# Kernel optimization log

Measured on AMD Instinct MI355X. Metric: run time of the kernel, lower is better.

The kernel has to match this reference:

```python
import jax, jax.numpy as jnp
import numpy as np

GRID = 32
SCALE_FACTOR = 0.2
EPS = 1e-12


def _compute_phi(verts, faces, G):
    """Unsigned distance-to-mesh on a GxGxG grid over [-1,1]^3, zeroed outside the mesh.
    Returns phi[z, y, x] (grid_sample D,H,W layout). verts [V,3], faces [F,3] int.
    Matches the SDF CUDA kernel semantics: phi = penetration depth (dist inside, 0 outside)."""
    v0 = verts[faces[:, 0]]  # [F,3]
    v1 = verts[faces[:, 1]]
    v2 = verts[faces[:, 2]]
    e0 = v1 - v0             # [F,3]
    e1 = v2 - v0
    a = jnp.sum(e0 * e0, -1)             # [F]
    b = jnp.sum(e0 * e1, -1)
    c = jnp.sum(e1 * e1, -1)

    lin = jnp.linspace(-1.0, 1.0, G, dtype=verts.dtype)
    zz, yy, xx = jnp.meshgrid(lin, lin, lin, indexing='ij')
    pts = jnp.stack([xx, yy, zz], -1).reshape(-1, 3)   # [P,3], coords (x,y,z), P=G^3

    # --- point-to-triangle squared distance, all [P,F] after one [P,F,3] temp ---
    w = pts[:, None, :] - v0[None, :, :]               # [P,F,3]
    f = jnp.sum(w * w, -1)                             # |p-v0|^2   [P,F]
    de0 = jnp.sum(w * e0, -1)                          # (p-v0).e0  [P,F]
    de1 = jnp.sum(w * e1, -1)                          # (p-v0).e1  [P,F]

    det = a * c - b * b                                # [F]
    det_s = jnp.where(det > EPS, det, 1.0)
    u = (c * de0 - b * de1) / det_s                    # barycentric of plane projection
    v = (a * de1 - b * de0) / det_s
    inside_tri = (u >= 0) & (v >= 0) & (u + v <= 1) & (det > EPS)
    plane_d2 = f - (u * de0 + v * de1)                 # squared dist to plane point

    # edge v0->v1
    a_s = jnp.where(a > EPS, a, 1.0)
    t0 = jnp.clip(de0 / a_s, 0.0, 1.0)
    d2_0 = f - 2.0 * t0 * de0 + t0 * t0 * a
    # edge v0->v2
    c_s = jnp.where(c > EPS, c, 1.0)
    t1 = jnp.clip(de1 / c_s, 0.0, 1.0)
    d2_1 = f - 2.0 * t1 * de1 + t1 * t1 * c
    # edge v1->v2: e2 = e1-e0; w1 = p - v1 = w - e0
    ee2 = a + c - 2.0 * b                              # |e2|^2
    ee2_s = jnp.where(ee2 > EPS, ee2, 1.0)
    dot2 = de1 - de0 - (b - a)                         # w1.e2
    w1sq = f - 2.0 * de0 + a                           # |w1|^2
    t2 = jnp.clip(dot2 / ee2_s, 0.0, 1.0)
    d2_2 = w1sq - 2.0 * t2 * dot2 + t2 * t2 * ee2

    edge_d2 = jnp.minimum(jnp.minimum(d2_0, d2_1), d2_2)
    d2 = jnp.where(inside_tri, plane_d2, edge_d2)
    d2 = jnp.maximum(d2, 0.0)
    dist = jnp.sqrt(jnp.min(d2, axis=1))               # [P]

    # --- inside/outside via +z ray casting parity ---
    x0, y0, z0 = v0[:, 0], v0[:, 1], v0[:, 2]
    x1, y1, z1 = v1[:, 0], v1[:, 1], v1[:, 2]
    x2, y2, z2 = v2[:, 0], v2[:, 1], v2[:, 2]
    det2 = (x1 - x0) * (y2 - y0) - (x2 - x0) * (y1 - y0)   # [F]
    det2_s = jnp.where(jnp.abs(det2) > EPS, det2, 1.0)
    px = pts[:, 0:1]; py = pts[:, 1:2]; pz = pts[:, 2:3]   # [P,1]
    u2 = ((px - x0) * (y2 - y0) - (py - y0) * (x2 - x0)) / det2_s  # [P,F]
    v2b = ((x1 - x0) * (py - y0) - (y1 - y0) * (px - x0)) / det2_s
    in2d = (u2 >= 0) & (v2b >= 0) & (u2 + v2b <= 1) & (jnp.abs(det2) > EPS)
    zint = z0 + u2 * (z1 - z0) + v2b * (z2 - z0)
    hits = jnp.sum((in2d & (zint > pz)).astype(jnp.int32), axis=1)  # [P]
    inside_mesh = (hits % 2).astype(dist.dtype)

    phi = dist * inside_mesh                           # >= 0 everywhere
    return phi.reshape(G, G, G)                        # [z, y, x]


def _trilinear_zeros(phi, q):
    """torch grid_sample(mode=bilinear, padding=zeros, align_corners=True) on a
    [G,G,G] (z,y,x) volume at points q [N,3] with coords (x,y,z) in [-1,1]."""
    G = phi.shape[0]
    fidx = (q + 1.0) * 0.5 * (G - 1)                   # [N,3] float indices (x,y,z)
    i0 = jnp.floor(fidx).astype(jnp.int32)
    w1 = fidx - i0.astype(fidx.dtype)
    w0 = 1.0 - w1
    out = jnp.zeros(q.shape[0], dtype=phi.dtype)
    for dz in (0, 1):
        for dy in (0, 1):
            for dx in (0, 1):
                ix = i0[:, 0] + dx
                iy = i0[:, 1] + dy
                iz = i0[:, 2] + dz
                valid = (ix >= 0) & (ix < G) & (iy >= 0) & (iy < G) & (iz >= 0) & (iz < G)
                val = phi[jnp.clip(iz, 0, G - 1), jnp.clip(iy, 0, G - 1), jnp.clip(ix, 0, G - 1)]
                wgt = ((w1[:, 0] if dx else w0[:, 0]) *
                       (w1[:, 1] if dy else w0[:, 1]) *
                       (w1[:, 2] if dz else w0[:, 2]))
                out = out + jnp.where(valid, val * wgt, 0.0)
    return out


def _sdf_loss(human_verts, object_verts, faces):
    sg = jax.lax.stop_gradient
    # bounding boxes (computed under no_grad in the original)
    bmin_h = jnp.min(human_verts, axis=0); bmax_h = jnp.max(human_verts, axis=0)
    bmin_o = jnp.min(object_verts, axis=0); bmax_o = jnp.max(object_verts, axis=0)
    overlap = jnp.all(bmin_h <= bmax_o) & jnp.all(bmin_o <= bmax_h)

    center = sg(0.5 * (bmin_h + bmax_h))                               # [3]
    scale = sg((1.0 + SCALE_FACTOR) * 0.5 * jnp.max(bmax_h - bmin_h))  # scalar

    hv_scaled = sg((human_verts - center) / scale)      # in [-1,1]^3 by construction
    phi = sg(_compute_phi(hv_scaled, faces, GRID))      # [G,G,G], no_grad in original

    q = (object_verts - center) / scale                 # grads flow to object_verts
    phi_val = _trilinear_zeros(phi, q)                  # [N]
    loss = jnp.sum(phi_val) ** 2
    return jnp.where(overlap, loss, jnp.zeros((), dtype=loss.dtype))


def setup_inputs() -> dict:
    key = jax.random.key(0)
    k1, k2, k3 = jax.random.split(key, 3)
    human_verts = jax.random.normal(k1, (778, 3), dtype=jnp.float32)
    object_verts = jax.random.normal(k2, (4096, 3), dtype=jnp.float32)
    faces = jax.random.randint(k3, (1538, 3), 0, 778, dtype=jnp.int32)
    return {"human_verts": human_verts, "object_verts": object_verts, "faces": faces}


def reference(human_verts, object_verts, faces):
    return _sdf_loss(human_verts, object_verts, faces)
```

## Files before the change

### kernel.cpp

```cpp
#include <hip/hip_runtime.h>

#define EPSF 1e-12f
#define GN 32
#define NPTS (GN * GN * GN)
#define NCOL (GN * GN)
#define FSPLIT 16
#define NCG 16
#define NBLK (NCG * FSPLIT)
#define NTHR 1024
#define MAXCH 160
#define CAP 8192
#define POISON 0xAAAAAAAAu

__device__ __forceinline__ float dot_rn(const float* x, const float* y) {
    return __fadd_rn(__fadd_rn(__fmul_rn(x[0], y[0]), __fmul_rn(x[1], y[1])),
                     __fmul_rn(x[2], y[2]));
}
__device__ __forceinline__ float wmin64(float v) {
    for (int o = 32; o > 0; o >>= 1) v = fminf(v, __shfl_xor(v, o));
    return v;
}
__device__ __forceinline__ float wmax64(float v) {
    for (int o = 32; o > 0; o >>= 1) v = fmaxf(v, __shfl_xor(v, o));
    return v;
}
__device__ __forceinline__ float wsum64(float v) {
    for (int o = 32; o > 0; o >>= 1) v += __shfl_xor(v, o);
    return v;
}
__device__ __forceinline__ float gridc(int g) {
    return __fadd_rn(-1.0f, __fmul_rn((float)g, 2.0f / 31.0f));
}
__device__ __forceinline__ int clampi(int v, int lo, int hi) {
    return v < lo ? lo : (v > hi ? hi : v);
}

__device__ __forceinline__ void frec(const float* __restrict__ hv,
                                     const int* __restrict__ faces, int f,
                                     float cx, float cy, float cz, float sc,
                                     float* o) {
    const float qnan = __int_as_float(0x7FC00000);
    int ia = faces[3 * f + 0], ib = faces[3 * f + 1], ic = faces[3 * f + 2];
    float v0[3], v1[3], v2[3];
    for (int k = 0; k < 3; ++k) {
        float cen = (k == 0) ? cx : ((k == 1) ? cy : cz);
        v0[k] = __fdiv_rn(__fsub_rn(hv[3 * ia + k], cen), sc);
        v1[k] = __fdiv_rn(__fsub_rn(hv[3 * ib + k], cen), sc);
        v2[k] = __fdiv_rn(__fsub_rn(hv[3 * ic + k], cen), sc);
    }
    float e0[3], e1[3];
    for (int k = 0; k < 3; ++k) {
        e0[k] = __fsub_rn(v1[k], v0[k]);
        e1[k] = __fsub_rn(v2[k], v0[k]);
    }
    float a = dot_rn(e0, e0);
    float b = dot_rn(e0, e1);
    float cc = dot_rn(e1, e1);
    float det = __fsub_rn(__fmul_rn(a, cc), __fmul_rn(b, b));
    float inv_det = (det > EPSF) ? (1.0f / det) : qnan;
    float inv_a = 1.0f / ((a > EPSF) ? a : 1.0f);
    float inv_c = 1.0f / ((cc > EPSF) ? cc : 1.0f);
    float ee2 = __fsub_rn(__fadd_rn(a, cc), __fmul_rn(2.0f, b));
    float inv_ee2 = 1.0f / ((ee2 > EPSF) ? ee2 : 1.0f);
    float det2 = __fsub_rn(__fmul_rn(e0[0], e1[1]), __fmul_rn(e1[0], e0[1]));
    float inv_det2s = (fabsf(det2) > EPSF) ? (1.0f / det2) : qnan;
    o[0] = v0[0]; o[1] = v0[1]; o[2] = v0[2];
    o[3] = e0[0]; o[4] = e0[1]; o[5] = e0[2];
    o[6] = e1[0]; o[7] = e1[1]; o[8] = e1[2];
    o[9] = a; o[10] = b; o[11] = cc;
    o[12] = inv_det; o[13] = inv_a; o[14] = inv_c;
    o[15] = ee2; o[16] = inv_ee2; o[17] = inv_det2s;
    o[18] = __fsub_rn(b, a); o[19] = 0.f;
}

__device__ __forceinline__ float celld2(const float* r, float px, float py, float pz) {
    float wx = __fsub_rn(px, r[0]), wy = __fsub_rn(py, r[1]), wz = __fsub_rn(pz, r[2]);
    float ff = wx * wx + wy * wy + wz * wz;
    float de0 = wx * r[3] + wy * r[4] + wz * r[5];
    float de1 = wx * r[6] + wy * r[7] + wz * r[8];
    float u = (r[11] * de0 - r[10] * de1) * r[12];
    float v = (r[9] * de1 - r[10] * de0) * r[12];
    bool inside = (u >= 0.0f) & (v >= 0.0f) & (u + v <= 1.0f);
    float plane_d2 = ff - (u * de0 + v * de1);
    float t0 = fminf(fmaxf(de0 * r[13], 0.0f), 1.0f);
    float d2_0 = ff + t0 * (t0 * r[9] - 2.0f * de0);
    float t1 = fminf(fmaxf(de1 * r[14], 0.0f), 1.0f);
    float d2_1 = ff + t1 * (t1 * r[11] - 2.0f * de1);
    float dot2 = (de1 - de0) - r[18];
    float w1sq = ff - 2.0f * de0 + r[9];
    float t2 = fminf(fmaxf(dot2 * r[16], 0.0f), 1.0f);
    float d2_2 = w1sq + t2 * (t2 * r[15] - 2.0f * dot2);
    float ed2 = fminf(fminf(d2_0, d2_1), d2_2);
    float d2 = inside ? plane_d2 : ed2;
    return fmaxf(d2, 0.0f);
}

__global__ void __launch_bounds__(NTHR) k_all(
    const float* __restrict__ hv, int nh,
    const float* __restrict__ ov, int no,
    const int* __restrict__ faces, int nf,
    unsigned* __restrict__ d2u, unsigned* __restrict__ parm,
    unsigned* __restrict__ counter, float* __restrict__ out)
{
    __shared__ float s_fd[MAXCH * 20];
    __shared__ unsigned s_sm[NCOL];
    __shared__ unsigned s_clist[CAP];
    __shared__ unsigned s_cnt[16];
    __shared__ unsigned s_pm[64];
    __shared__ float s_w[16][12];
    __shared__ float s_hdr[4];
    __shared__ float s_hb[6];
    __shared__ float s_ovl;
    __shared__ unsigned s_last;

    int t = threadIdx.x, lane = t & 63, wvid = t >> 6;
    int fs = blockIdx.x >> 4;
    int cg = blockIdx.x & 15;
    const float step = 2.0f / 31.0f;

    for (int i = t; i < NCOL; i += NTHR) s_sm[i] = 0u;
    if (t < 64) s_pm[t] = 0u;

    {
        float mnx = INFINITY, mny = INFINITY, mnz = INFINITY;
        float mxx = -INFINITY, mxy = -INFINITY, mxz = -INFINITY;
        for (int i = t; i < nh; i += NTHR) {
            float x = hv[3 * i], y = hv[3 * i + 1], z = hv[3 * i + 2];
            mnx = fminf(mnx, x); mny = fminf(mny, y); mnz = fminf(mnz, z);
            mxx = fmaxf(mxx, x); mxy = fmaxf(mxy, y); mxz = fmaxf(mxz, z);
        }
        mnx = wmin64(mnx); mny = wmin64(mny); mnz = wmin64(mnz);
        mxx = wmax64(mxx); mxy = wmax64(mxy); mxz = wmax64(mxz);
        if (lane == 0) {
            s_w[wvid][0] = mnx; s_w[wvid][1] = mny; s_w[wvid][2] = mnz;
            s_w[wvid][3] = mxx; s_w[wvid][4] = mxy; s_w[wvid][5] = mxz;
        }
        __syncthreads();
        if (wvid == 0) {
            float a0 = (lane < 16) ? s_w[lane][0] : INFINITY;
            float a1 = (lane < 16) ? s_w[lane][1] : INFINITY;
            float a2 = (lane < 16) ? s_w[lane][2] : INFINITY;
            float a3 = (lane < 16) ? s_w[lane][3] : -INFINITY;
            float a4 = (lane < 16) ? s_w[lane][4] : -INFINITY;
            float a5 = (lane < 16) ? s_w[lane][5] : -INFINITY;
            a0 = wmin64(a0); a1 = wmin64(a1); a2 = wmin64(a2);
            a3 = wmax64(a3); a4 = wmax64(a4); a5 = wmax64(a5);
            if (lane == 0) {
                float e0 = __fsub_rn(a3, a0);
                float e1 = __fsub_rn(a4, a1);
                float e2 = __fsub_rn(a5, a2);
                float m = fmaxf(e0, fmaxf(e1, e2));
                s_hdr[0] = __fmul_rn(0.5f, __fadd_rn(a0, a3));
                s_hdr[1] = __fmul_rn(0.5f, __fadd_rn(a1, a4));
                s_hdr[2] = __fmul_rn(0.5f, __fadd_rn(a2, a5));
                s_hdr[3] = __fmul_rn(0.6f, m);
                s_hb[0] = a0; s_hb[1] = a1; s_hb[2] = a2;
                s_hb[3] = a3; s_hb[4] = a4; s_hb[5] = a5;
            }
        }
        __syncthreads();
    }
    float cx = s_hdr[0], cy = s_hdr[1], cz = s_hdr[2], sc = s_hdr[3];

    int chunkB = (nf + FSPLIT - 1) / FSPLIT;
    int f0B = fs * chunkB;
    int nloc = min(nf, f0B + chunkB) - f0B;
    for (int i = t; i < nloc; i += NTHR)
        frec(hv, faces, f0B + i, cx, cy, cz, sc, s_fd + i * 20);
    {
        float onx = INFINITY, ony = INFINITY, onz = INFINITY;
        float oxx = -INFINITY, oxy = -INFINITY, oxz = -INFINITY;
        for (int j = t; j < no; j += NTHR) {
            float x = ov[3 * j + 0], y = ov[3 * j + 1], z = ov[3 * j + 2];
            onx = fminf(onx, x); ony = fminf(ony, y); onz = fminf(onz, z);
            oxx = fmaxf(oxx, x); oxy = fmaxf(oxy, y); oxz = fmaxf(oxz, z);
            float qx = __fdiv_rn(__fsub_rn(x, cx), sc);
            float qy = __fdiv_rn(__fsub_rn(y, cy), sc);
            float qz = __fdiv_rn(__fsub_rn(z, cz), sc);
            float fx = __fmul_rn(__fmul_rn(__fadd_rn(qx, 1.0f), 0.5f), 31.0f);
            float fy = __fmul_rn(__fmul_rn(__fadd_rn(qy, 1.0f), 0.5f), 31.0f);
            float fz = __fmul_rn(__fmul_rn(__fadd_rn(qz, 1.0f), 0.5f), 31.0f);
            int ix0 = (int)floorf(fx), iy0 = (int)floorf(fy), iz0 = (int)floorf(fz);
            unsigned zb = 0u;
            if ((iz0 >= 0) & (iz0 < GN)) zb |= 1u << iz0;
            if ((iz0 + 1 >= 0) & (iz0 + 1 < GN)) zb |= 1u << (iz0 + 1);
            if (zb) {
                for (int dy = 0; dy < 2; ++dy)
                    for (int dx = 0; dx < 2; ++dx) {
                        int ix = ix0 + dx, iy = iy0 + dy;
                        if ((ix >= 0) & (ix < GN) & (iy >= 0) & (iy < GN))
                            atomicOr(&s_sm[iy * GN + ix], zb);
                    }
            }
        }
        onx = wmin64(onx); ony = wmin64(ony); onz = wmin64(onz);
        oxx = wmax64(oxx); oxy = wmax64(oxy); oxz = wmax64(oxz);
        if (lane == 0) {
            s_w[wvid][6] = onx; s_w[wvid][7] = ony; s_w[wvid][8] = onz;
            s_w[wvid][9] = oxx; s_w[wvid][10] = oxy; s_w[wvid][11] = oxz;
        }
    }
    __syncthreads();
    if (t == 0) {
        float a0 = INFINITY, a1 = INFINITY, a2 = INFINITY;
        float a3 = -INFINITY, a4 = -INFINITY, a5 = -INFINITY;
        for (int wv = 0; wv < 16; ++wv) {
            a0 = fminf(a0, s_w[wv][6]); a1 = fminf(a1, s_w[wv][7]);
            a2 = fminf(a2, s_w[wv][8]); a3 = fmaxf(a3, s_w[wv][9]);
            a4 = fmaxf(a4, s_w[wv][10]); a5 = fmaxf(a5, s_w[wv][11]);
        }
        bool ovl = (s_hb[0] <= a3) && (s_hb[1] <= a4) && (s_hb[2] <= a5) &&
                   (a0 <= s_hb[3]) && (a1 <= s_hb[4]) && (a2 <= s_hb[5]);
        s_ovl = ovl ? 1.0f : 0.0f;
    }

    {
        int col = cg * 64 + lane;
        int gx = col & 31, gy = col >> 5;
        float px = __fadd_rn(-1.0f, __fmul_rn((float)gx, step));
        float py = __fadd_rn(-1.0f, __fmul_rn((float)gy, step));
        int i0 = __builtin_amdgcn_readfirstlane((wvid * nloc) / 16);
        int i1 = __builtin_amdgcn_readfirstlane(((wvid + 1) * nloc) / 16);

        unsigned cmask = 0u;
        for (int i = i0; i < i1; ++i) {
            const float* q = s_fd + i * 20;
            float v0x = q[0], v0y = q[1], v0z = q[2];
            float e0x = q[3], e0y = q[4], e0z = q[5];
            float e1x = q[6], e1y = q[7], e1z = q[8];
            float inv_det2s = q[17];

            float wx = __fsub_rn(px, v0x), wy = __fsub_rn(py, v0y);
            float u2n = __fsub_rn(__fmul_rn(wx, e1y), __fmul_rn(wy, e1x));
            float v2n = __fsub_rn(__fmul_rn(e0x, wy), __fmul_rn(e0y, wx));
            float u2 = __fmul_rn(u2n, inv_det2s);
            float v2 = __fmul_rn(v2n, inv_det2s);
            bool in2d = (u2 >= 0.0f) & (v2 >= 0.0f) & (__fadd_rn(u2, v2) <= 1.0f);
            float zint = __fadd_rn(__fadd_rn(v0z, __fmul_rn(u2, e0z)), __fmul_rn(v2, e1z));
            int c = 0;
            {
                float p;
                p = __fadd_rn(-1.0f, __fmul_rn((float)(15), step));      if (zint > p) c = 16;
                p = __fadd_rn(-1.0f, __fmul_rn((float)(c + 7), step));   if (zint > p) c += 8;
                p = __fadd_rn(-1.0f, __fmul_rn((float)(c + 3), step));   if (zint > p) c += 4;
                p = __fadd_rn(-1.0f, __fmul_rn((float)(c + 1), step));   if (zint > p) c += 2;
                p = __fadd_rn(-1.0f, __fmul_rn((float)(c), step));       if (zint > p) c += 1;
                p = __fadd_rn(-1.0f, __fmul_rn((float)(c), step));       if (zint > p) c += 1;
            }
            unsigned mask = (c == 0) ? 0u : (0xffffffffu >> (32 - c));
            cmask ^= in2d ? mask : 0u;
        }
        atomicXor(&s_pm[lane], cmask);
        __syncthreads();
        if (t < 64) atomicXor(&parm[cg * 64 + t], s_pm[t]);
    }

    unsigned nc;
    {
        unsigned cnt = 0;
        for (int chunk = wvid * 32; chunk < wvid * 32 + 32; ++chunk) {
            unsigned cid = (unsigned)(chunk * 64 + lane);
            bool present = (s_sm[cid >> 5] >> (cid & 31u)) & 1u;
            cnt += (unsigned)__popcll(__ballot(present));
        }
        if (lane == 0) s_cnt[wvid] = cnt;
        __syncthreads();
        unsigned base = 0;
        for (int wv = 0; wv < wvid; ++wv) base += s_cnt[wv];
        nc = base;
        for (int wv = wvid; wv < 16; ++wv) nc += s_cnt[wv];
        if (nc <= CAP) {
            for (int chunk = wvid * 32; chunk < wvid * 32 + 32; ++chunk) {
                unsigned cid = (unsigned)(chunk * 64 + lane);
                bool present = (s_sm[cid >> 5] >> (cid & 31u)) & 1u;
                unsigned long long bal = __ballot(present);
                unsigned pre = (unsigned)__popcll(bal & ((1ull << lane) - 1ull));
                if (present) s_clist[base + pre] = cid;
                base += (unsigned)__popcll(bal);
            }
        }
        __syncthreads();
    }

    {
        bool uselist = nc <= CAP;
        unsigned nbatch = uselist ? ((nc + 63) >> 6) : (NPTS / 64);
        for (unsigned cb = (unsigned)cg + 16u * (unsigned)wvid; cb < nbatch;
             cb += 256u) {
            unsigned idx = cb * 64 + (unsigned)lane;
            bool cvalid; unsigned cid;
            if (uselist) { cvalid = idx < nc; cid = cvalid ? s_clist[idx] : 0u; }
            else { cid = idx; cvalid = (s_sm[cid >> 5] >> (cid & 31u)) & 1u; }
            int gx = (int)((cid >> 5) & 31u), gy = (int)(cid >> 10),
                gz = (int)(cid & 31u);
            float px = gridc(gx), py = gridc(gy), pz = gridc(gz);
            float dmin = 3.402823466e38f;
            for (int i = 0; i < nloc; ++i)
                dmin = fminf(dmin, celld2(s_fd + i * 20, px, py, pz));
            if (cvalid) atomicMin(&d2u[cid], __float_as_uint(dmin));
        }
    }

    __syncthreads();
    if (t == 0) {
        unsigned old = atomicAdd(counter, 1u);
        s_last = (old == POISON + (unsigned)(NBLK - 1)) ? 1u : 0u;
    }
    __syncthreads();
    if (s_last == 0u) return;

    {
        float ovl = s_ovl;
        s_sm[t] = __hip_atomic_load(&parm[t], __ATOMIC_RELAXED,
                                    __HIP_MEMORY_SCOPE_AGENT) ^ POISON;
        __syncthreads();
        float acc = 0.0f;
        for (int j = t; j < no; j += NTHR) {
            float qx = __fdiv_rn(__fsub_rn(ov[3 * j + 0], cx), sc);
            float qy = __fdiv_rn(__fsub_rn(ov[3 * j + 1], cy), sc);
            float qz = __fdiv_rn(__fsub_rn(ov[3 * j + 2], cz), sc);
            float fx = __fmul_rn(__fmul_rn(__fadd_rn(qx, 1.0f), 0.5f), 31.0f);
            float fy = __fmul_rn(__fmul_rn(__fadd_rn(qy, 1.0f), 0.5f), 31.0f);
            float fz = __fmul_rn(__fmul_rn(__fadd_rn(qz, 1.0f), 0.5f), 31.0f);
            float flx = floorf(fx), fly = floorf(fy), flz = floorf(fz);
            int ix0 = (int)flx, iy0 = (int)fly, iz0 = (int)flz;
            float w1x = __fsub_rn(fx, flx), w0x = __fsub_rn(1.0f, w1x);
            float w1y = __fsub_rn(fy, fly), w0y = __fsub_rn(1.0f, w1y);
            float w1z = __fsub_rn(fz, flz), w0z = __fsub_rn(1.0f, w1z);
            int xc0 = clampi(ix0, 0, 31), xc1 = clampi(ix0 + 1, 0, 31);
            int yc0 = clampi(iy0, 0, 31), yc1 = clampi(iy0 + 1, 0, 31);
            int zc0 = clampi(iz0, 0, 31), zc1 = clampi(iz0 + 1, 0, 31);
            unsigned du[8];
#pragma unroll
            for (int k = 0; k < 8; ++k) {
                int xx = (k & 1) ? xc1 : xc0;
                int yy = ((k >> 1) & 1) ? yc1 : yc0;
                int zz = (k >> 2) ? zc1 : zc0;
                du[k] = __hip_atomic_load(&d2u[(yy * GN + xx) * GN + zz],
                            __ATOMIC_RELAXED, __HIP_MEMORY_SCOPE_AGENT);
            }
            for (int dy = 0; dy < 2; ++dy)
                for (int dx = 0; dx < 2; ++dx) {
                    int ix = ix0 + dx, iy = iy0 + dy;
                    bool okxy = (ix >= 0) & (ix < GN) & (iy >= 0) & (iy < GN);
                    unsigned pm = okxy ? s_sm[iy * GN + ix] : 0u;
                    for (int dz = 0; dz < 2; ++dz) {
                        int iz = iz0 + dz;
                        bool ok = okxy & (iz >= 0) & (iz < GN);
                        if (ok && ((pm >> iz) & 1u)) {
                            float val = sqrtf(__uint_as_float(du[dz * 4 + dy * 2 + dx]));
                            float wgt = __fmul_rn(
                                __fmul_rn(dx ? w1x : w0x, dy ? w1y : w0y),
                                dz ? w1z : w0z);
                            acc = __fadd_rn(acc, __fmul_rn(val, wgt));
                        }
                    }
                }
        }
        acc = wsum64(acc);
        if (lane == 0) s_w[wvid][0] = acc;
        __syncthreads();
        if (wvid == 0) {
            float v = (lane < 16) ? s_w[lane][0] : 0.0f;
            v = wsum64(v);
            if (lane == 0) {
                float loss = __fmul_rn(v, v);
                out[0] = (ovl != 0.0f) ? loss : 0.0f;
            }
        }
    }
}

extern "C" void kernel_launch(void* const* d_in, const int* in_sizes, int n_in,
                              void* d_out, int out_size, void* d_ws, size_t ws_size,
                              hipStream_t stream) {
    const float* hv = (const float*)d_in[0];
    const float* ov = (const float*)d_in[1];
    const int* faces = (const int*)d_in[2];
    int nh = in_sizes[0] / 3;
    int no = in_sizes[1] / 3;
    int nf = in_sizes[2] / 3;

    unsigned* d2u = (unsigned*)d_ws;
    unsigned* parm = d2u + NPTS;
    unsigned* counter = parm + NCOL;

    k_all<<<NBLK, NTHR, 0, stream>>>(hv, nh, ov, no, faces, nf,
                                     d2u, parm, counter, (float*)d_out);
}
```

Before: 112.5 us.

## Split face chunk across waves per cell batch and reduce minima in LDS

Each wave used to own whole batches of 64 cells and loop over every face in the block's chunk. Now all 16 waves work on the same cell batch, each taking one sixteenth of the faces. Partial minima are combined with LDS atomicMin, then written to global memory with one atomicMin per cell. The aim is to balance work across waves when there are few cell batches, and to cut global atomics. The cost is extra block-wide barriers per group of eight batches, plus LDS atomic traffic.

```diff
diff --git a/kernel.cpp b/kernel.cpp
--- a/kernel.cpp
+++ b/kernel.cpp
@@ -10,6 +10,7 @@
 #define NTHR 1024
 #define MAXCH 160
 #define CAP 8192
+#define LB 8
 #define POISON 0xAAAAAAAAu
 
 __device__ __forceinline__ float dot_rn(const float* x, const float* y) {
@@ -107,6 +108,7 @@
     __shared__ unsigned s_clist[CAP];
     __shared__ unsigned s_cnt[16];
     __shared__ unsigned s_pm[64];
+    __shared__ unsigned s_dm[LB * 64];
     __shared__ float s_w[16][12];
     __shared__ float s_hdr[4];
     __shared__ float s_hb[6];
@@ -285,19 +287,44 @@
     {
         bool uselist = nc <= CAP;
         unsigned nbatch = uselist ? ((nc + 63) >> 6) : (NPTS / 64);
-        for (unsigned cb = (unsigned)cg + 16u * (unsigned)wvid; cb < nbatch;
-             cb += 256u) {
-            unsigned idx = cb * 64 + (unsigned)lane;
-            bool cvalid; unsigned cid;
-            if (uselist) { cvalid = idx < nc; cid = cvalid ? s_clist[idx] : 0u; }
-            else { cid = idx; cvalid = (s_sm[cid >> 5] >> (cid & 31u)) & 1u; }
-            int gx = (int)((cid >> 5) & 31u), gy = (int)(cid >> 10),
-                gz = (int)(cid & 31u);
-            float px = gridc(gx), py = gridc(gy), pz = gridc(gz);
-            float dmin = 3.402823466e38f;
-            for (int i = 0; i < nloc; ++i)
-                dmin = fminf(dmin, celld2(s_fd + i * 20, px, py, pz));
-            if (cvalid) atomicMin(&d2u[cid], __float_as_uint(dmin));
+        unsigned nlb = (nbatch > (unsigned)cg)
+                           ? ((nbatch - (unsigned)cg + 15u) >> 4) : 0u;
+        int i0 = __builtin_amdgcn_readfirstlane((wvid * nloc) / 16);
+        int i1 = __builtin_amdgcn_readfirstlane(((wvid + 1) * nloc) / 16);
+
+        for (unsigned k0 = 0; k0 < nlb; k0 += LB) {
+            unsigned ke = min(nlb, k0 + LB);
+            unsigned nk = ke - k0;
+            for (int i = t; i < (int)(nk * 64u); i += NTHR)
+                s_dm[i] = 0x7f800000u;
+            __syncthreads();
+            for (unsigned k = k0; k < ke; ++k) {
+                unsigned cb = (unsigned)cg + (k << 4);
+                unsigned idx = cb * 64 + (unsigned)lane;
+                bool cvalid; unsigned cid;
+                if (uselist) { cvalid = idx < nc; cid = cvalid ? s_clist[idx] : 0u; }
+                else { cid = idx; cvalid = (s_sm[cid >> 5] >> (cid & 31u)) & 1u; }
+                int gx = (int)((cid >> 5) & 31u), gy = (int)(cid >> 10),
+                    gz = (int)(cid & 31u);
+                float px = gridc(gx), py = gridc(gy), pz = gridc(gz);
+                float dmin = 3.402823466e38f;
+                for (int i = i0; i < i1; ++i)
+                    dmin = fminf(dmin, celld2(s_fd + i * 20, px, py, pz));
+                if (cvalid)
+                    atomicMin(&s_dm[(k - k0) * 64 + (unsigned)lane],
+                              __float_as_uint(dmin));
+            }
+            __syncthreads();
+            for (int i = t; i < (int)(nk * 64u); i += NTHR) {
+                unsigned k = k0 + (unsigned)(i >> 6);
+                unsigned cb = (unsigned)cg + (k << 4);
+                unsigned idx2 = cb * 64 + (unsigned)(i & 63);
+                bool v2; unsigned c2;
+                if (uselist) { v2 = idx2 < nc; c2 = v2 ? s_clist[idx2] : 0u; }
+                else { c2 = idx2; v2 = (s_sm[c2 >> 5] >> (c2 & 31u)) & 1u; }
+                if (v2) atomicMin(&d2u[c2], s_dm[i]);
+            }
+            __syncthreads();
         }
     }
 
```

Result: faster. 110.3 us (-2.0%).

## Split faces across waves with LDS min-reduce; distribute trilinear tail over all blocks

Applied to the files above, without the earlier changes.

In the distance phase, each wave now takes a slice of the block's face chunk instead of a separate batch of grid cells. The per-cell minima are combined with LDS atomics and a single global atomicMin per cell, which reduces global atomic traffic but adds two block barriers per batch. The old last-block tail is replaced by a grid-wide spin barrier, after which every block samples its share of object points and accumulates into a global float sum. A second counter finalises the loss. This spreads the serial sampling tail across blocks, but it relies on all 256 blocks being co-resident and makes the float summation order nondeterministic.

```diff
diff --git a/kernel.cpp b/kernel.cpp
--- a/kernel.cpp
+++ b/kernel.cpp
@@ -100,18 +100,19 @@
     const float* __restrict__ ov, int no,
     const int* __restrict__ faces, int nf,
     unsigned* __restrict__ d2u, unsigned* __restrict__ parm,
-    unsigned* __restrict__ counter, float* __restrict__ out)
+    unsigned* __restrict__ counter, unsigned* __restrict__ counter2,
+    float* __restrict__ gsum, float* __restrict__ out)
 {
     __shared__ float s_fd[MAXCH * 20];
     __shared__ unsigned s_sm[NCOL];
     __shared__ unsigned s_clist[CAP];
     __shared__ unsigned s_cnt[16];
     __shared__ unsigned s_pm[64];
+    __shared__ unsigned s_dm[64];
     __shared__ float s_w[16][12];
     __shared__ float s_hdr[4];
     __shared__ float s_hb[6];
     __shared__ float s_ovl;
-    __shared__ unsigned s_last;
 
     int t = threadIdx.x, lane = t & 63, wvid = t >> 6;
     int fs = blockIdx.x >> 4;
@@ -285,8 +286,12 @@
     {
         bool uselist = nc <= CAP;
         unsigned nbatch = uselist ? ((nc + 63) >> 6) : (NPTS / 64);
-        for (unsigned cb = (unsigned)cg + 16u * (unsigned)wvid; cb < nbatch;
-             cb += 256u) {
+        int i0 = __builtin_amdgcn_readfirstlane((wvid * nloc) / 16);
+        int i1 = __builtin_amdgcn_readfirstlane(((wvid + 1) * nloc) / 16);
+
+        for (unsigned cb = (unsigned)cg; cb < nbatch; cb += 16) {
+            if (t < 64) s_dm[t] = 0x7f800000u;
+            __syncthreads();
             unsigned idx = cb * 64 + (unsigned)lane;
             bool cvalid; unsigned cid;
             if (uselist) { cvalid = idx < nc; cid = cvalid ? s_clist[idx] : 0u; }
@@ -295,77 +300,98 @@
                 gz = (int)(cid & 31u);
             float px = gridc(gx), py = gridc(gy), pz = gridc(gz);
             float dmin = 3.402823466e38f;
-            for (int i = 0; i < nloc; ++i)
+            for (int i = i0; i < i1; ++i)
                 dmin = fminf(dmin, celld2(s_fd + i * 20, px, py, pz));
-            if (cvalid) atomicMin(&d2u[cid], __float_as_uint(dmin));
+            if (cvalid) atomicMin(&s_dm[lane], __float_as_uint(dmin));
+            __syncthreads();
+            if (t < 64) {
+                unsigned idx2 = cb * 64 + (unsigned)t;
+                bool v2; unsigned c2;
+                if (uselist) { v2 = idx2 < nc; c2 = v2 ? s_clist[idx2] : 0u; }
+                else { c2 = idx2; v2 = (s_sm[c2 >> 5] >> (c2 & 31u)) & 1u; }
+                if (v2) atomicMin(&d2u[c2], s_dm[t]);
+            }
+            __syncthreads();
         }
     }
 
     __syncthreads();
     if (t == 0) {
-        unsigned old = atomicAdd(counter, 1u);
-        s_last = (old == POISON + (unsigned)(NBLK - 1)) ? 1u : 0u;
+        atomicAdd(counter, 1u);
+        unsigned target = POISON + (unsigned)NBLK;
+        while (__hip_atomic_load(counter, __ATOMIC_ACQUIRE,
+                                 __HIP_MEMORY_SCOPE_AGENT) != target)
+            __builtin_amdgcn_s_sleep(8);
     }
     __syncthreads();
-    if (s_last == 0u) return;
-
-    {
-        float ovl = s_ovl;
-        s_sm[t] = __hip_atomic_load(&parm[t], __ATOMIC_RELAXED,
-                                    __HIP_MEMORY_SCOPE_AGENT) ^ POISON;
-        __syncthreads();
+
+    {
         float acc = 0.0f;
-        for (int j = t; j < no; j += NTHR) {
-            float qx = __fdiv_rn(__fsub_rn(ov[3 * j + 0], cx), sc);
-            float qy = __fdiv_rn(__fsub_rn(ov[3 * j + 1], cy), sc);
-            float qz = __fdiv_rn(__fsub_rn(ov[3 * j + 2], cz), sc);
-            float fx = __fmul_rn(__fmul_rn(__fadd_rn(qx, 1.0f), 0.5f), 31.0f);
-            float fy = __fmul_rn(__fmul_rn(__fadd_rn(qy, 1.0f), 0.5f), 31.0f);
-            float fz = __fmul_rn(__fmul_rn(__fadd_rn(qz, 1.0f), 0.5f), 31.0f);
-            float flx = floorf(fx), fly = floorf(fy), flz = floorf(fz);
-            int ix0 = (int)flx, iy0 = (int)fly, iz0 = (int)flz;
-            float w1x = __fsub_rn(fx, flx), w0x = __fsub_rn(1.0f, w1x);
-            float w1y = __fsub_rn(fy, fly), w0y = __fsub_rn(1.0f, w1y);
-            float w1z = __fsub_rn(fz, flz), w0z = __fsub_rn(1.0f, w1z);
-            int xc0 = clampi(ix0, 0, 31), xc1 = clampi(ix0 + 1, 0, 31);
-            int yc0 = clampi(iy0, 0, 31), yc1 = clampi(iy0 + 1, 0, 31);
-            int zc0 = clampi(iz0, 0, 31), zc1 = clampi(iz0 + 1, 0, 31);
-            unsigned du[8];
+        int npb = (no + NBLK - 1) / NBLK;
+        if (wvid == 0) {
+            int j = blockIdx.x * npb + lane;
+            if (lane < npb && j < no) {
+                float qx = __fdiv_rn(__fsub_rn(ov[3 * j + 0], cx), sc);
+                float qy = __fdiv_rn(__fsub_rn(ov[3 * j + 1], cy), sc);
+                float qz = __fdiv_rn(__fsub_rn(ov[3 * j + 2], cz), sc);
+                float fx = __fmul_rn(__fmul_rn(__fadd_rn(qx, 1.0f), 0.5f), 31.0f);
+                float fy = __fmul_rn(__fmul_rn(__fadd_rn(qy, 1.0f), 0.5f), 31.0f);
+                float fz = __fmul_rn(__fmul_rn(__fadd_rn(qz, 1.0f), 0.5f), 31.0f);
+                float flx = floorf(fx), fly = floorf(fy), flz = floorf(fz);
+                int ix0 = (int)flx, iy0 = (int)fly, iz0 = (int)flz;
+                float w1x = __fsub_rn(fx, flx), w0x = __fsub_rn(1.0f, w1x);
+                float w1y = __fsub_rn(fy, fly), w0y = __fsub_rn(1.0f, w1y);
+                float w1z = __fsub_rn(fz, flz), w0z = __fsub_rn(1.0f, w1z);
+                int xc0 = clampi(ix0, 0, 31), xc1 = clampi(ix0 + 1, 0, 31);
+                int yc0 = clampi(iy0, 0, 31), yc1 = clampi(iy0 + 1, 0, 31);
+                int zc0 = clampi(iz0, 0, 31), zc1 = clampi(iz0 + 1, 0, 31);
+                unsigned du[8];
 #pragma unroll
-            for (int k = 0; k < 8; ++k) {
-                int xx = (k & 1) ? xc1 : xc0;
-                int yy = ((k >> 1) & 1) ? yc1 : yc0;
-                int zz = (k >> 2) ? zc1 : zc0;
-                du[k] = __hip_atomic_load(&d2u[(yy * GN + xx) * GN + zz],
-                            __ATOMIC_RELAXED, __HIP_MEMORY_SCOPE_AGENT);
-            }
-            for (int dy = 0; dy < 2; ++dy)
-                for (int dx = 0; dx < 2; ++dx) {
-                    int ix = ix0 + dx, iy = iy0 + dy;
-                    bool okxy = (ix >= 0) & (ix < GN) & (iy >= 0) & (iy < GN);
-                    unsigned pm = okxy ? s_sm[iy * GN + ix] : 0u;
-                    for (int dz = 0; dz < 2; ++dz) {
-                        int iz = iz0 + dz;
-                        bool ok = okxy & (iz >= 0) & (iz < GN);
-                        if (ok && ((pm >> iz) & 1u)) {
-                            float val = sqrtf(__uint_as_float(du[dz * 4 + dy * 2 + dx]));
-                            float wgt = __fmul_rn(
-                                __fmul_rn(dx ? w1x : w0x, dy ? w1y : w0y),
-                                dz ? w1z : w0z);
-                            acc = __fadd_rn(acc, __fmul_rn(val, wgt));
+                for (int k = 0; k < 8; ++k) {
+                    int xx = (k & 1) ? xc1 : xc0;
+                    int yy = ((k >> 1) & 1) ? yc1 : yc0;
+                    int zz = (k >> 2) ? zc1 : zc0;
+                    du[k] = __hip_atomic_load(&d2u[(yy * GN + xx) * GN + zz],
+                                __ATOMIC_RELAXED, __HIP_MEMORY_SCOPE_AGENT);
+                }
+                unsigned pmv[4];
+#pragma unroll
+                for (int k = 0; k < 4; ++k) {
+                    int xx = (k & 1) ? xc1 : xc0;
+                    int yy = (k >> 1) ? yc1 : yc0;
+                    pmv[k] = __hip_atomic_load(&parm[yy * GN + xx],
+                                 __ATOMIC_RELAXED, __HIP_MEMORY_SCOPE_AGENT) ^ POISON;
+                }
+                for (int dy = 0; dy < 2; ++dy)
+                    for (int dx = 0; dx < 2; ++dx) {
+                        int ix = ix0 + dx, iy = iy0 + dy;
+                        bool okxy = (ix >= 0) & (ix < GN) & (iy >= 0) & (iy < GN);
+                        unsigned pm = okxy ? pmv[dy * 2 + dx] : 0u;
+                        for (int dz = 0; dz < 2; ++dz) {
+                            int iz = iz0 + dz;
+                            bool ok = okxy & (iz >= 0) & (iz < GN);
+                            if (ok && ((pm >> iz) & 1u)) {
+                                float val = sqrtf(__uint_as_float(du[dz * 4 + dy * 2 + dx]));
+                                float wgt = __fmul_rn(
+                                    __fmul_rn(dx ? w1x : w0x, dy ? w1y : w0y),
+                                    dz ? w1z : w0z);
+                                acc = __fadd_rn(acc, __fmul_rn(val, wgt));
+                            }
                         }
                     }
+            }
+            acc = wsum64(acc);
+            if (lane == 0) {
+                float oldg = atomicAdd(gsum, acc);
+                unsigned dep = (unsigned)(oldg * 0.0f);
+                unsigned old2 = __hip_atomic_fetch_add(counter2, 1u + dep,
+                                    __ATOMIC_ACQ_REL, __HIP_MEMORY_SCOPE_AGENT);
+                if (old2 == POISON + (unsigned)(NBLK - 1)) {
+                    float S = __hip_atomic_load(gsum, __ATOMIC_ACQUIRE,
+                                                __HIP_MEMORY_SCOPE_AGENT);
+                    float loss = __fmul_rn(S, S);
+                    out[0] = (s_ovl != 0.0f) ? loss : 0.0f;
                 }
-        }
-        acc = wsum64(acc);
-        if (lane == 0) s_w[wvid][0] = acc;
-        __syncthreads();
-        if (wvid == 0) {
-            float v = (lane < 16) ? s_w[lane][0] : 0.0f;
-            v = wsum64(v);
-            if (lane == 0) {
-                float loss = __fmul_rn(v, v);
-                out[0] = (ovl != 0.0f) ? loss : 0.0f;
             }
         }
     }
@@ -384,7 +410,10 @@
     unsigned* d2u = (unsigned*)d_ws;
     unsigned* parm = d2u + NPTS;
     unsigned* counter = parm + NCOL;
+    unsigned* counter2 = counter + 1;
+    float* gsum = (float*)(counter + 2);
 
     k_all<<<NBLK, NTHR, 0, stream>>>(hv, nh, ov, no, faces, nf,
-                                     d2u, parm, counter, (float*)d_out);
-}
+                                     d2u, parm, counter, counter2, gsum,
+                                     (float*)d_out);
+}
```

After: 104.3 us. 7.3% less time.
